# Kernel optimization log

Measured on AMD Instinct MI355X. Metric: run time of the kernel, lower is better.

## Reference

```python
import jax, jax.numpy as jnp
import numpy as np

B, L, NSTATE = 8192, 256, 9


def setup_inputs() -> dict:
    key = jax.random.key(0)
    k1, k2, k3, k4 = jax.random.split(key, 4)
    inputs = jax.random.normal(k1, (B, L, NSTATE), dtype=jnp.float32)
    path = jax.random.randint(k2, (B, L), 0, NSTATE, dtype=jnp.int32)
    # learned CRF params (init'd to zeros in the module; use small random for a
    # non-degenerate reference)
    tran = jax.random.normal(k3, (NSTATE, NSTATE), dtype=jnp.float32) * 0.1
    init = jax.random.normal(k4, (NSTATE,), dtype=jnp.float32) * 0.1
    return {"inputs": inputs, "path": path, "tran": tran, "init": init}


def reference(inputs, path, tran, init):
    # inputs: [B, L, S], path: [B, L], tran: [S, S], init: [S]
    # bio=False -> mask and imask are all zeros (no-op additions).
    # --- gold path score ---
    emit = jnp.take_along_axis(inputs, path[..., None], axis=-1)[..., 0]  # [B, L]
    tran_sc = tran[path[..., :-1], path[..., 1:]]                         # [B, L-1]
    path_scores = emit.sum(-1) + init[path[..., 0]] + tran_sc.sum(-1)     # [B]

    # --- partition function via log-semiring forward recurrence ---
    alpha0 = init + inputs[..., 0, :]                                     # [B, S]

    def step(alpha, x_t):
        # alpha: [B, S] (prev state), x_t: [B, S] (emission at t)
        nxt = alpha[..., :, None] + tran + x_t[..., None, :]              # [B, S, S]
        return jax.nn.logsumexp(nxt, axis=-2), None

    xs = jnp.moveaxis(inputs[..., 1:, :], -2, 0)                          # [L-1, B, S]
    alpha, _ = jax.lax.scan(step, alpha0, xs)
    scores = jax.nn.logsumexp(alpha, axis=-1)                             # [B]
    return scores - path_scores
```

## Files before the change

kernel.cpp:

```cpp
#include <hip/hip_runtime.h>


#define B_N 8192
#define L_N 256
#define SEQ_STRIDE 2304
#define HALF 128
#define SPB 6
#define XW 54
#define XSTRIDE 55
#define NBLK 22
#define PLS 129
#define SPW 16
#define NDIR_BLOCKS (B_N / SPW)

#define LOG2E 1.44269504088896340736f
#define LN2f  0.69314718055994530942f

#define QP1 57
#define QP2 78
#define QP3 147
#define QROT(src, CTRL) \
  __int_as_float(__builtin_amdgcn_mov_dpp(__float_as_int(src), CTRL, 0xf, 0xf, 0))

__device__ __forceinline__ void gl_lds4(const void* g, void* l) {
  __builtin_amdgcn_global_load_lds(
      (const __attribute__((address_space(1))) void*)g,
      (__attribute__((address_space(3))) void*)l, 4, 0, 0);
}

__device__ __forceinline__ float fexp(float x) {
  return __builtin_amdgcn_exp2f(x * LOG2E);
}

__global__ __launch_bounds__(64, 1) void crf_half(
    const float* __restrict__ xg, const int* __restrict__ path,
    const float* __restrict__ tran, const float* __restrict__ initv,
    float* __restrict__ ws)
{
  __shared__ float lx[2][SPW * XSTRIDE];
  __shared__ int   pl[SPW * PLS];
  __shared__ int   pl255[SPW];
  __shared__ float ltran[81];

  const int lane = threadIdx.x;
  const int c = lane & 3;
  const int q = lane >> 2;
  const bool fwd = (int)blockIdx.x < NDIR_BLOCKS;
  const int seq0 = (fwd ? blockIdx.x : blockIdx.x - NDIR_BLOCKS) * SPW;

  for (int i = lane; i < 81; i += 64) ltran[i] = tran[i];

  {
    const int t0 = fwd ? 0 : 127;
#pragma unroll
    for (int r = 0; r < SPW; ++r) {
      const int* g = path + (size_t)(seq0 + r) * L_N + t0 + lane;
      gl_lds4(g,      &pl[r * PLS]);
      gl_lds4(g + 64, &pl[r * PLS + 64]);
    }
  }
  if (!fwd && lane < SPW)
    pl255[lane] = path[(size_t)(seq0 + lane) * L_N + 255];

  if (lane < XW) {
    const int fb = fwd ? 0 : (SEQ_STRIDE - XW);
#pragma unroll
    for (int r = 0; r < SPW; ++r)
      gl_lds4(xg + (size_t)(seq0 + r) * SEQ_STRIDE + fb + lane,
              &lx[0][r * XSTRIDE]);
  }

  float Erot[4][3][3];
#pragma unroll
  for (int r = 0; r < 4; ++r)
#pragma unroll
    for (int k = 0; k < 3; ++k)
#pragma unroll
      for (int i = 0; i < 3; ++i) {
        const int ig = 3 * c + i;
        const int jg = 3 * ((c + r) & 3) + k;
        float v = 0.f;
        if (ig < 9 && jg < 9)
          v = fexp(fwd ? tran[jg * 9 + ig] : tran[ig * 9 + jg]);
        Erot[r][k][i] = v;
      }

  float o[3];
  float emit = 0.f, trn = 0.f;
  int ce = 0, pcur = 0;

  if (!fwd) {
#pragma unroll
    for (int k = 0; k < 3; ++k) o[k] = (c < 3) ? 1.f : 0.f;
    pcur = pl255[q];
  }

  const int myoff = (c == 3) ? 0 : 3 * c;

#pragma unroll 1
  for (int b = 0; b < NBLK; ++b) {
    asm volatile("s_waitcnt vmcnt(0)" ::: "memory");

    if (b + 1 < NBLK && lane < XW) {
      const int fb = fwd ? (b + 1) * XW : (SEQ_STRIDE - XW * (b + 2));
      float* dst = &lx[(b + 1) & 1][0];
#pragma unroll
      for (int r = 0; r < SPW; ++r)
        gl_lds4(xg + (size_t)(seq0 + r) * SEQ_STRIDE + fb + lane,
                dst + r * XSTRIDE);
    }

    const float* lxq = &lx[b & 1][q * XSTRIDE];

    float e[SPB * 3];
#pragma unroll
    for (int tt = 0; tt < SPB; ++tt)
#pragma unroll
      for (int k = 0; k < 3; ++k)
        e[tt * 3 + k] = fexp(lxq[tt * 9 + myoff + k]);

    if (fwd) {
#pragma unroll
      for (int kk = 0; kk < SPB; ++kk) {
        const int t = b * SPB + kk;
        if (t < HALF) {
          if (t == 0) {
#pragma unroll
            for (int k = 0; k < 3; ++k)
              o[k] = (c < 3) ? fexp(initv[3 * c + k] + lxq[myoff + k]) : 0.f;
            pcur = pl[q * PLS];
            emit = lxq[pcur];
          } else {
            float g[4][3];
#pragma unroll
            for (int k = 0; k < 3; ++k) {
              g[0][k] = o[k];
              g[1][k] = QROT(o[k], QP1);
              g[2][k] = QROT(o[k], QP2);
              g[3][k] = QROT(o[k], QP3);
            }
            if (kk == 0 && b > 0) {
              float m = g[0][0];
#pragma unroll
              for (int r = 0; r < 4; ++r)
#pragma unroll
                for (int k = 0; k < 3; ++k) m = fmaxf(m, g[r][k]);
              const int ex = (int)((__float_as_uint(m) >> 23) & 0xffu) - 126;
              ce += ex;
              const float sc = __uint_as_float((unsigned)(127 - ex) << 23);
#pragma unroll
              for (int r = 0; r < 4; ++r)
#pragma unroll
                for (int k = 0; k < 3; ++k) g[r][k] *= sc;
            }
            float out[3];
#pragma unroll
            for (int i = 0; i < 3; ++i) {
              float a = Erot[0][0][i] * g[0][0];
#pragma unroll
              for (int r = 0; r < 4; ++r)
#pragma unroll
                for (int k = 0; k < 3; ++k)
                  if (r + k > 0) a = fmaf(Erot[r][k][i], g[r][k], a);
              out[i] = a;
            }
            const int p = pl[q * PLS + t];
            emit += lxq[kk * 9 + p];
            trn  += ltran[pcur * 9 + p];
            pcur = p;
#pragma unroll
            for (int i = 0; i < 3; ++i) o[i] = out[i] * e[kk * 3 + i];
          }
        }
      }
    } else {
#pragma unroll
      for (int kk = 0; kk < SPB; ++kk) {
        const int t = 255 - b * SPB - kk;
        if (t >= HALF) {
          const int tt = SPB - 1 - kk;
          float w[3];
#pragma unroll
          for (int k = 0; k < 3; ++k) w[k] = e[tt * 3 + k] * o[k];
          float g[4][3];
#pragma unroll
          for (int k = 0; k < 3; ++k) {
            g[0][k] = w[k];
            g[1][k] = QROT(w[k], QP1);
            g[2][k] = QROT(w[k], QP2);
            g[3][k] = QROT(w[k], QP3);
          }
          if (kk == 0 && b > 0) {
            float m = g[0][0];
#pragma unroll
            for (int r = 0; r < 4; ++r)
#pragma unroll
              for (int k = 0; k < 3; ++k) m = fmaxf(m, g[r][k]);
            const int ex = (int)((__float_as_uint(m) >> 23) & 0xffu) - 126;
            ce += ex;
            const float sc = __uint_as_float((unsigned)(127 - ex) << 23);
#pragma unroll
            for (int r = 0; r < 4; ++r)
#pragma unroll
              for (int k = 0; k < 3; ++k) g[r][k] *= sc;
          }
#pragma unroll
          for (int i = 0; i < 3; ++i) {
            float a = Erot[0][0][i] * g[0][0];
#pragma unroll
            for (int r = 0; r < 4; ++r)
#pragma unroll
              for (int k = 0; k < 3; ++k)
                if (r + k > 0) a = fmaf(Erot[r][k][i], g[r][k], a);
            o[i] = a;
          }
          emit += lxq[tt * 9 + pcur];
          const int pm = pl[q * PLS + (t - 1 - 127)];
          trn += ltran[pm * 9 + pcur];
          pcur = pm;
        }
      }
    }
  }

  const int sq = seq0 + q;
  float* wp = ws + sq;
  if (fwd) {
    if (c < 3) {
#pragma unroll
      for (int k = 0; k < 3; ++k) wp[(3 * c + k) * B_N] = o[k];
    } else {
      wp[9 * B_N] = (float)ce;
      const int p0 = pl[q * PLS];
      wp[10 * B_N] = emit + trn + initv[p0];
    }
  } else {
    if (c < 3) {
#pragma unroll
      for (int k = 0; k < 3; ++k) wp[(11 + 3 * c + k) * B_N] = o[k];
    } else {
      wp[20 * B_N] = (float)ce;
      wp[21 * B_N] = emit + trn;
    }
  }
}

__global__ __launch_bounds__(256) void crf_combine(
    const float* __restrict__ ws, float* __restrict__ out)
{
  const int s = blockIdx.x * 256 + threadIdx.x;
  float dot = 0.f;
#pragma unroll
  for (int i = 0; i < 9; ++i)
    dot = fmaf(ws[i * B_N + s], ws[(11 + i) * B_N + s], dot);
  const float score =
      (__builtin_amdgcn_logf(dot) + ws[9 * B_N + s] + ws[20 * B_N + s]) * LN2f;
  out[s] = score - (ws[10 * B_N + s] + ws[21 * B_N + s]);
}

extern "C" void kernel_launch(void* const* d_in, const int* in_sizes, int n_in,
                              void* d_out, int out_size, void* d_ws, size_t ws_size,
                              hipStream_t stream) {
  (void)in_sizes; (void)n_in; (void)out_size; (void)ws_size;
  const float* xg    = (const float*)d_in[0];
  const int*   path  = (const int*)d_in[1];
  const float* tran  = (const float*)d_in[2];
  const float* initv = (const float*)d_in[3];
  float* ws  = (float*)d_ws;
  float* out = (float*)d_out;

  crf_half<<<2 * NDIR_BLOCKS, 64, 0, stream>>>(xg, path, tran, initv, ws);
  crf_combine<<<B_N / 256, 256, 0, stream>>>(ws, out);
}
```

Before: 133.8 us.

## Fuse forward/backward halves and combine into one kernel with triple-buffered prefetch

Each block now runs two wavefronts, one doing the forward half and one the backward half of the same 16 sequences. The halves are combined through shared memory, which removes the second combine kernel and the workspace round trip. The emission prefetch goes from double to triple buffering, with partial vmcnt waits so loads stay in flight two blocks ahead. The cost is more LDS per block and a block-wide barrier at the end, and the hand-counted vmcnt values must match the number of outstanding loads.

After: 145.5 us. 1.09x slower.

```diff
diff --git a/kernel.cpp b/kernel.cpp
--- a/kernel.cpp
+++ b/kernel.cpp
@@ -11,7 +11,7 @@
 #define NBLK 22
 #define PLS 129
 #define SPW 16
-#define NDIR_BLOCKS (B_N / SPW)
+#define NBLOCKS (B_N / SPW)
 
 #define LOG2E 1.44269504088896340736f
 #define LN2f  0.69314718055994530942f
@@ -22,6 +22,8 @@
 #define QROT(src, CTRL) \
   __int_as_float(__builtin_amdgcn_mov_dpp(__float_as_int(src), CTRL, 0xf, 0xf, 0))
 
+#define WAITV(N) asm volatile("s_waitcnt vmcnt(" #N ")" ::: "memory")
+
 __device__ __forceinline__ void gl_lds4(const void* g, void* l) {
   __builtin_amdgcn_global_load_lds(
       (const __attribute__((address_space(1))) void*)g,
@@ -32,43 +34,25 @@
   return __builtin_amdgcn_exp2f(x * LOG2E);
 }
 
-__global__ __launch_bounds__(64, 1) void crf_half(
+__global__ __launch_bounds__(128, 1) void crf_fused(
     const float* __restrict__ xg, const int* __restrict__ path,
     const float* __restrict__ tran, const float* __restrict__ initv,
-    float* __restrict__ ws)
+    float* __restrict__ out)
 {
-  __shared__ float lx[2][SPW * XSTRIDE];
-  __shared__ int   pl[SPW * PLS];
-  __shared__ int   pl255[SPW];
-  __shared__ float ltran[81];
-
-  const int lane = threadIdx.x;
+  __shared__ float lx[2][3][SPW * XSTRIDE];
+  __shared__ int   pl[2][SPW * PLS];
+  __shared__ float ltran[2][81];
+  __shared__ float comb[2][SPW][11];
+
+  const int tid  = threadIdx.x;
+  const int w    = tid >> 6;
+  const int lane = tid & 63;
   const int c = lane & 3;
   const int q = lane >> 2;
-  const bool fwd = (int)blockIdx.x < NDIR_BLOCKS;
-  const int seq0 = (fwd ? blockIdx.x : blockIdx.x - NDIR_BLOCKS) * SPW;
-
-  for (int i = lane; i < 81; i += 64) ltran[i] = tran[i];
-
-  {
-    const int t0 = fwd ? 0 : 127;
-#pragma unroll
-    for (int r = 0; r < SPW; ++r) {
-      const int* g = path + (size_t)(seq0 + r) * L_N + t0 + lane;
-      gl_lds4(g,      &pl[r * PLS]);
-      gl_lds4(g + 64, &pl[r * PLS + 64]);
-    }
-  }
-  if (!fwd && lane < SPW)
-    pl255[lane] = path[(size_t)(seq0 + lane) * L_N + 255];
-
-  if (lane < XW) {
-    const int fb = fwd ? 0 : (SEQ_STRIDE - XW);
-#pragma unroll
-    for (int r = 0; r < SPW; ++r)
-      gl_lds4(xg + (size_t)(seq0 + r) * SEQ_STRIDE + fb + lane,
-              &lx[0][r * XSTRIDE]);
-  }
+  const bool fwd = (w == 0);
+  const int seq0 = blockIdx.x * SPW;
+
+  for (int i = lane; i < 81; i += 64) ltran[w][i] = tran[i];
 
   float Erot[4][3][3];
 #pragma unroll
@@ -85,32 +69,63 @@
         Erot[r][k][i] = v;
       }
 
+  float iv[3];
+#pragma unroll
+  for (int k = 0; k < 3; ++k) {
+    iv[k] = (fwd && c < 3) ? initv[3 * c + k] : 0.f;
+    asm volatile("" :: "v"(iv[k]));
+  }
+
   float o[3];
   float emit = 0.f, trn = 0.f;
   int ce = 0, pcur = 0;
-
   if (!fwd) {
 #pragma unroll
     for (int k = 0; k < 3; ++k) o[k] = (c < 3) ? 1.f : 0.f;
-    pcur = pl255[q];
-  }
-
+    pcur = path[(size_t)(seq0 + q) * L_N + 255];
+  }
+  asm volatile("" :: "v"(pcur));
   const int myoff = (c == 3) ? 0 : 3 * c;
+
+  {
+    const int t0 = fwd ? 0 : 127;
+#pragma unroll
+    for (int r = 0; r < SPW; ++r) {
+      const int* g = path + (size_t)(seq0 + r) * L_N + t0 + lane;
+      gl_lds4(g,      &pl[w][r * PLS]);
+      gl_lds4(g + 64, &pl[w][r * PLS + 64]);
+    }
+  }
+  if (lane < XW) {
+#pragma unroll
+    for (int wi = 0; wi < 2; ++wi) {
+      const int fb = fwd ? wi * XW : (SEQ_STRIDE - XW * (wi + 1));
+#pragma unroll
+      for (int r = 0; r < SPW; ++r)
+        gl_lds4(xg + (size_t)(seq0 + r) * SEQ_STRIDE + fb + lane,
+                &lx[w][wi][r * XSTRIDE]);
+    }
+  }
 
 #pragma unroll 1
   for (int b = 0; b < NBLK; ++b) {
-    asm volatile("s_waitcnt vmcnt(0)" ::: "memory");
-
-    if (b + 1 < NBLK && lane < XW) {
-      const int fb = fwd ? (b + 1) * XW : (SEQ_STRIDE - XW * (b + 2));
-      float* dst = &lx[(b + 1) & 1][0];
-#pragma unroll
-      for (int r = 0; r < SPW; ++r)
-        gl_lds4(xg + (size_t)(seq0 + r) * SEQ_STRIDE + fb + lane,
-                dst + r * XSTRIDE);
-    }
-
-    const float* lxq = &lx[b & 1][q * XSTRIDE];
+    if (b + 2 < NBLK) {
+      if (lane < XW) {
+        const int fb = fwd ? (b + 2) * XW : (SEQ_STRIDE - XW * (b + 3));
+        float* dst = &lx[w][(b + 2) % 3][0];
+#pragma unroll
+        for (int r = 0; r < SPW; ++r)
+          gl_lds4(xg + (size_t)(seq0 + r) * SEQ_STRIDE + fb + lane,
+                  dst + r * XSTRIDE);
+      }
+      WAITV(32);
+    } else if (b + 1 < NBLK) {
+      WAITV(16);
+    } else {
+      WAITV(0);
+    }
+
+    const float* lxq = &lx[w][b % 3][q * XSTRIDE];
 
     float e[SPB * 3];
 #pragma unroll
@@ -127,8 +142,8 @@
           if (t == 0) {
 #pragma unroll
             for (int k = 0; k < 3; ++k)
-              o[k] = (c < 3) ? fexp(initv[3 * c + k] + lxq[myoff + k]) : 0.f;
-            pcur = pl[q * PLS];
+              o[k] = (c < 3) ? fexp(iv[k] + lxq[myoff + k]) : 0.f;
+            pcur = pl[w][q * PLS];
             emit = lxq[pcur];
           } else {
             float g[4][3];
@@ -153,7 +168,7 @@
 #pragma unroll
                 for (int k = 0; k < 3; ++k) g[r][k] *= sc;
             }
-            float out[3];
+            float out3[3];
 #pragma unroll
             for (int i = 0; i < 3; ++i) {
               float a = Erot[0][0][i] * g[0][0];
@@ -162,14 +177,14 @@
 #pragma unroll
                 for (int k = 0; k < 3; ++k)
                   if (r + k > 0) a = fmaf(Erot[r][k][i], g[r][k], a);
-              out[i] = a;
+              out3[i] = a;
             }
-            const int p = pl[q * PLS + t];
+            const int p = pl[w][q * PLS + t];
             emit += lxq[kk * 9 + p];
-            trn  += ltran[pcur * 9 + p];
+            trn  += ltran[w][pcur * 9 + p];
             pcur = p;
 #pragma unroll
-            for (int i = 0; i < 3; ++i) o[i] = out[i] * e[kk * 3 + i];
+            for (int i = 0; i < 3; ++i) o[i] = out3[i] * e[kk * 3 + i];
           }
         }
       }
@@ -179,16 +194,16 @@
         const int t = 255 - b * SPB - kk;
         if (t >= HALF) {
           const int tt = SPB - 1 - kk;
-          float w[3];
-#pragma unroll
-          for (int k = 0; k < 3; ++k) w[k] = e[tt * 3 + k] * o[k];
+          float wv[3];
+#pragma unroll
+          for (int k = 0; k < 3; ++k) wv[k] = e[tt * 3 + k] * o[k];
           float g[4][3];
 #pragma unroll
           for (int k = 0; k < 3; ++k) {
-            g[0][k] = w[k];
-            g[1][k] = QROT(w[k], QP1);
-            g[2][k] = QROT(w[k], QP2);
-            g[3][k] = QROT(w[k], QP3);
+            g[0][k] = wv[k];
+            g[1][k] = QROT(wv[k], QP1);
+            g[2][k] = QROT(wv[k], QP2);
+            g[3][k] = QROT(wv[k], QP3);
           }
           if (kk == 0 && b > 0) {
             float m = g[0][0];
@@ -215,60 +230,44 @@
             o[i] = a;
           }
           emit += lxq[tt * 9 + pcur];
-          const int pm = pl[q * PLS + (t - 1 - 127)];
-          trn += ltran[pm * 9 + pcur];
+          const int pm = pl[w][q * PLS + (t - 1 - 127)];
+          trn += ltran[w][pm * 9 + pcur];
           pcur = pm;
         }
       }
     }
   }
 
-  const int sq = seq0 + q;
-  float* wp = ws + sq;
-  if (fwd) {
-    if (c < 3) {
-#pragma unroll
-      for (int k = 0; k < 3; ++k) wp[(3 * c + k) * B_N] = o[k];
-    } else {
-      wp[9 * B_N] = (float)ce;
-      const int p0 = pl[q * PLS];
-      wp[10 * B_N] = emit + trn + initv[p0];
-    }
+  if (c < 3) {
+#pragma unroll
+    for (int k = 0; k < 3; ++k) comb[w][q][3 * c + k] = o[k];
   } else {
-    if (c < 3) {
-#pragma unroll
-      for (int k = 0; k < 3; ++k) wp[(11 + 3 * c + k) * B_N] = o[k];
-    } else {
-      wp[20 * B_N] = (float)ce;
-      wp[21 * B_N] = emit + trn;
-    }
-  }
-}
-
-__global__ __launch_bounds__(256) void crf_combine(
-    const float* __restrict__ ws, float* __restrict__ out)
-{
-  const int s = blockIdx.x * 256 + threadIdx.x;
-  float dot = 0.f;
-#pragma unroll
-  for (int i = 0; i < 9; ++i)
-    dot = fmaf(ws[i * B_N + s], ws[(11 + i) * B_N + s], dot);
-  const float score =
-      (__builtin_amdgcn_logf(dot) + ws[9 * B_N + s] + ws[20 * B_N + s]) * LN2f;
-  out[s] = score - (ws[10 * B_N + s] + ws[21 * B_N + s]);
+    comb[w][q][9]  = (float)ce;
+    comb[w][q][10] = fwd ? (emit + trn + initv[pl[w][q * PLS]])
+                         : (emit + trn);
+  }
+  __syncthreads();
+
+  if (tid < SPW) {
+    float dot = 0.f;
+#pragma unroll
+    for (int i = 0; i < 9; ++i)
+      dot = fmaf(comb[0][tid][i], comb[1][tid][i], dot);
+    const float score =
+        (__builtin_amdgcn_logf(dot) + comb[0][tid][9] + comb[1][tid][9]) * LN2f;
+    out[seq0 + tid] = score - (comb[0][tid][10] + comb[1][tid][10]);
+  }
 }
 
 extern "C" void kernel_launch(void* const* d_in, const int* in_sizes, int n_in,
                               void* d_out, int out_size, void* d_ws, size_t ws_size,
                               hipStream_t stream) {
-  (void)in_sizes; (void)n_in; (void)out_size; (void)ws_size;
+  (void)in_sizes; (void)n_in; (void)out_size; (void)d_ws; (void)ws_size;
   const float* xg    = (const float*)d_in[0];
   const int*   path  = (const int*)d_in[1];
   const float* tran  = (const float*)d_in[2];
   const float* initv = (const float*)d_in[3];
-  float* ws  = (float*)d_ws;
   float* out = (float*)d_out;
 
-  crf_half<<<2 * NDIR_BLOCKS, 64, 0, stream>>>(xg, path, tran, initv, ws);
-  crf_combine<<<B_N / 256, 256, 0, stream>>>(ws, out);
-}
+  crf_fused<<<NBLOCKS, 128, 0, stream>>>(xg, path, tran, initv, out);
+}
```

## Map one sequence per lane with full 9x9 matvec instead of DPP quad split

Applied to the files above, without the earlier changes.

Changes the work mapping from four lanes per sequence (exchanging 3-state slices via DPP quad rotations) to one lane per sequence holding all 9 states and the full 9x9 exp-transition matrix in registers. Each wave now handles 64 sequences, so the grid shrinks fourfold and the LDS staging buffers grow accordingly. This removes the DPP cross-lane traffic and the idle fourth lane per quad. In exchange it raises register pressure (81 matrix entries plus state vectors), lengthens the per-lane serial dependency chain, and leaves fewer blocks to hide latency, with more LDS per block.

Result: slower. 158.6 us (+18.5%).

```diff
diff --git a/kernel.cpp b/kernel.cpp
--- a/kernel.cpp
+++ b/kernel.cpp
@@ -10,17 +10,13 @@
 #define XSTRIDE 55
 #define NBLK 22
 #define PLS 129
-#define SPW 16
+#define SPW 64
 #define NDIR_BLOCKS (B_N / SPW)
 
 #define LOG2E 1.44269504088896340736f
 #define LN2f  0.69314718055994530942f
 
-#define QP1 57
-#define QP2 78
-#define QP3 147
-#define QROT(src, CTRL) \
-  __int_as_float(__builtin_amdgcn_mov_dpp(__float_as_int(src), CTRL, 0xf, 0xf, 0))
+#define WAITV0 asm volatile("s_waitcnt vmcnt(0)" ::: "memory")
 
 __device__ __forceinline__ void gl_lds4(const void* g, void* l) {
   __builtin_amdgcn_global_load_lds(
@@ -39,137 +35,109 @@
 {
   __shared__ float lx[2][SPW * XSTRIDE];
   __shared__ int   pl[SPW * PLS];
-  __shared__ int   pl255[SPW];
   __shared__ float ltran[81];
 
   const int lane = threadIdx.x;
-  const int c = lane & 3;
-  const int q = lane >> 2;
   const bool fwd = (int)blockIdx.x < NDIR_BLOCKS;
   const int seq0 = (fwd ? blockIdx.x : blockIdx.x - NDIR_BLOCKS) * SPW;
 
   for (int i = lane; i < 81; i += 64) ltran[i] = tran[i];
 
+  float E[9][9];
+#pragma unroll
+  for (int i = 0; i < 9; ++i)
+#pragma unroll
+    for (int j = 0; j < 9; ++j)
+      E[i][j] = fexp(fwd ? tran[j * 9 + i] : tran[i * 9 + j]);
+
+  float iv[9];
+#pragma unroll
+  for (int j = 0; j < 9; ++j) iv[j] = initv[j];
+
+  float a[9];
+  float emit = 0.f, trn = 0.f;
+  int ce = 0, pcur = 0;
+  if (!fwd) {
+#pragma unroll
+    for (int j = 0; j < 9; ++j) a[j] = 1.f;
+    pcur = path[(size_t)(seq0 + lane) * L_N + 255];
+  }
+  asm volatile("" :: "v"(pcur));
+
   {
     const int t0 = fwd ? 0 : 127;
-#pragma unroll
+#pragma unroll 4
     for (int r = 0; r < SPW; ++r) {
       const int* g = path + (size_t)(seq0 + r) * L_N + t0 + lane;
       gl_lds4(g,      &pl[r * PLS]);
       gl_lds4(g + 64, &pl[r * PLS + 64]);
     }
   }
-  if (!fwd && lane < SPW)
-    pl255[lane] = path[(size_t)(seq0 + lane) * L_N + 255];
-
   if (lane < XW) {
     const int fb = fwd ? 0 : (SEQ_STRIDE - XW);
-#pragma unroll
+#pragma unroll 4
     for (int r = 0; r < SPW; ++r)
       gl_lds4(xg + (size_t)(seq0 + r) * SEQ_STRIDE + fb + lane,
               &lx[0][r * XSTRIDE]);
   }
 
-  float Erot[4][3][3];
-#pragma unroll
-  for (int r = 0; r < 4; ++r)
-#pragma unroll
-    for (int k = 0; k < 3; ++k)
-#pragma unroll
-      for (int i = 0; i < 3; ++i) {
-        const int ig = 3 * c + i;
-        const int jg = 3 * ((c + r) & 3) + k;
-        float v = 0.f;
-        if (ig < 9 && jg < 9)
-          v = fexp(fwd ? tran[jg * 9 + ig] : tran[ig * 9 + jg]);
-        Erot[r][k][i] = v;
-      }
-
-  float o[3];
-  float emit = 0.f, trn = 0.f;
-  int ce = 0, pcur = 0;
-
-  if (!fwd) {
-#pragma unroll
-    for (int k = 0; k < 3; ++k) o[k] = (c < 3) ? 1.f : 0.f;
-    pcur = pl255[q];
-  }
-
-  const int myoff = (c == 3) ? 0 : 3 * c;
+  const int* plr = &pl[lane * PLS];
 
 #pragma unroll 1
   for (int b = 0; b < NBLK; ++b) {
-    asm volatile("s_waitcnt vmcnt(0)" ::: "memory");
+    WAITV0;
 
     if (b + 1 < NBLK && lane < XW) {
       const int fb = fwd ? (b + 1) * XW : (SEQ_STRIDE - XW * (b + 2));
       float* dst = &lx[(b + 1) & 1][0];
-#pragma unroll
+#pragma unroll 4
       for (int r = 0; r < SPW; ++r)
         gl_lds4(xg + (size_t)(seq0 + r) * SEQ_STRIDE + fb + lane,
                 dst + r * XSTRIDE);
     }
 
-    const float* lxq = &lx[b & 1][q * XSTRIDE];
-
-    float e[SPB * 3];
-#pragma unroll
-    for (int tt = 0; tt < SPB; ++tt)
-#pragma unroll
-      for (int k = 0; k < 3; ++k)
-        e[tt * 3 + k] = fexp(lxq[tt * 9 + myoff + k]);
+    const float* lxr = &lx[b & 1][lane * XSTRIDE];
 
     if (fwd) {
 #pragma unroll
       for (int kk = 0; kk < SPB; ++kk) {
         const int t = b * SPB + kk;
         if (t < HALF) {
+          float xv[9], ee[9];
+#pragma unroll
+          for (int j = 0; j < 9; ++j) xv[j] = lxr[kk * 9 + j];
+#pragma unroll
+          for (int j = 0; j < 9; ++j) ee[j] = fexp(xv[j]);
           if (t == 0) {
 #pragma unroll
-            for (int k = 0; k < 3; ++k)
-              o[k] = (c < 3) ? fexp(initv[3 * c + k] + lxq[myoff + k]) : 0.f;
-            pcur = pl[q * PLS];
-            emit = lxq[pcur];
+            for (int j = 0; j < 9; ++j) a[j] = fexp(iv[j] + xv[j]);
+            pcur = plr[0];
+            emit += lxr[pcur];
           } else {
-            float g[4][3];
-#pragma unroll
-            for (int k = 0; k < 3; ++k) {
-              g[0][k] = o[k];
-              g[1][k] = QROT(o[k], QP1);
-              g[2][k] = QROT(o[k], QP2);
-              g[3][k] = QROT(o[k], QP3);
-            }
             if (kk == 0 && b > 0) {
-              float m = g[0][0];
-#pragma unroll
-              for (int r = 0; r < 4; ++r)
-#pragma unroll
-                for (int k = 0; k < 3; ++k) m = fmaxf(m, g[r][k]);
+              float m = a[0];
+#pragma unroll
+              for (int j = 1; j < 9; ++j) m = fmaxf(m, a[j]);
               const int ex = (int)((__float_as_uint(m) >> 23) & 0xffu) - 126;
               ce += ex;
               const float sc = __uint_as_float((unsigned)(127 - ex) << 23);
 #pragma unroll
-              for (int r = 0; r < 4; ++r)
-#pragma unroll
-                for (int k = 0; k < 3; ++k) g[r][k] *= sc;
+              for (int j = 0; j < 9; ++j) a[j] *= sc;
             }
-            float out[3];
-#pragma unroll
-            for (int i = 0; i < 3; ++i) {
-              float a = Erot[0][0][i] * g[0][0];
-#pragma unroll
-              for (int r = 0; r < 4; ++r)
-#pragma unroll
-                for (int k = 0; k < 3; ++k)
-                  if (r + k > 0) a = fmaf(Erot[r][k][i], g[r][k], a);
-              out[i] = a;
+            float outv[9];
+#pragma unroll
+            for (int i = 0; i < 9; ++i) {
+              float acc = E[i][0] * a[0];
+#pragma unroll
+              for (int j = 1; j < 9; ++j) acc = fmaf(E[i][j], a[j], acc);
+              outv[i] = acc;
             }
-            const int p = pl[q * PLS + t];
-            emit += lxq[kk * 9 + p];
+            const int p = plr[t];
+            emit += lxr[kk * 9 + p];
             trn  += ltran[pcur * 9 + p];
             pcur = p;
 #pragma unroll
-            for (int i = 0; i < 3; ++i) o[i] = out[i] * e[kk * 3 + i];
+            for (int i = 0; i < 9; ++i) a[i] = outv[i] * ee[i];
           }
         }
       }
@@ -179,69 +147,54 @@
         const int t = 255 - b * SPB - kk;
         if (t >= HALF) {
           const int tt = SPB - 1 - kk;
-          float w[3];
-#pragma unroll
-          for (int k = 0; k < 3; ++k) w[k] = e[tt * 3 + k] * o[k];
-          float g[4][3];
-#pragma unroll
-          for (int k = 0; k < 3; ++k) {
-            g[0][k] = w[k];
-            g[1][k] = QROT(w[k], QP1);
-            g[2][k] = QROT(w[k], QP2);
-            g[3][k] = QROT(w[k], QP3);
-          }
+          float xv[9], ee[9], wv[9];
+#pragma unroll
+          for (int j = 0; j < 9; ++j) xv[j] = lxr[tt * 9 + j];
+#pragma unroll
+          for (int j = 0; j < 9; ++j) ee[j] = fexp(xv[j]);
+#pragma unroll
+          for (int j = 0; j < 9; ++j) wv[j] = ee[j] * a[j];
           if (kk == 0 && b > 0) {
-            float m = g[0][0];
-#pragma unroll
-            for (int r = 0; r < 4; ++r)
-#pragma unroll
-              for (int k = 0; k < 3; ++k) m = fmaxf(m, g[r][k]);
+            float m = wv[0];
+#pragma unroll
+            for (int j = 1; j < 9; ++j) m = fmaxf(m, wv[j]);
             const int ex = (int)((__float_as_uint(m) >> 23) & 0xffu) - 126;
             ce += ex;
             const float sc = __uint_as_float((unsigned)(127 - ex) << 23);
 #pragma unroll
-            for (int r = 0; r < 4; ++r)
-#pragma unroll
-              for (int k = 0; k < 3; ++k) g[r][k] *= sc;
+            for (int j = 0; j < 9; ++j) wv[j] *= sc;
           }
-#pragma unroll
-          for (int i = 0; i < 3; ++i) {
-            float a = Erot[0][0][i] * g[0][0];
-#pragma unroll
-            for (int r = 0; r < 4; ++r)
-#pragma unroll
-              for (int k = 0; k < 3; ++k)
-                if (r + k > 0) a = fmaf(Erot[r][k][i], g[r][k], a);
-            o[i] = a;
+          float outv[9];
+#pragma unroll
+          for (int i = 0; i < 9; ++i) {
+            float acc = E[i][0] * wv[0];
+#pragma unroll
+            for (int j = 1; j < 9; ++j) acc = fmaf(E[i][j], wv[j], acc);
+            outv[i] = acc;
           }
-          emit += lxq[tt * 9 + pcur];
-          const int pm = pl[q * PLS + (t - 1 - 127)];
+          emit += lxr[tt * 9 + pcur];
+          const int pm = plr[t - 128];
           trn += ltran[pm * 9 + pcur];
           pcur = pm;
+#pragma unroll
+          for (int i = 0; i < 9; ++i) a[i] = outv[i];
         }
       }
     }
   }
 
-  const int sq = seq0 + q;
+  const int sq = seq0 + lane;
   float* wp = ws + sq;
   if (fwd) {
-    if (c < 3) {
-#pragma unroll
-      for (int k = 0; k < 3; ++k) wp[(3 * c + k) * B_N] = o[k];
-    } else {
-      wp[9 * B_N] = (float)ce;
-      const int p0 = pl[q * PLS];
-      wp[10 * B_N] = emit + trn + initv[p0];
-    }
+#pragma unroll
+    for (int i = 0; i < 9; ++i) wp[i * B_N] = a[i];
+    wp[9 * B_N] = (float)ce;
+    wp[10 * B_N] = emit + trn + initv[plr[0]];
   } else {
-    if (c < 3) {
-#pragma unroll
-      for (int k = 0; k < 3; ++k) wp[(11 + 3 * c + k) * B_N] = o[k];
-    } else {
-      wp[20 * B_N] = (float)ce;
-      wp[21 * B_N] = emit + trn;
-    }
+#pragma unroll
+    for (int i = 0; i < 9; ++i) wp[(11 + i) * B_N] = a[i];
+    wp[20 * B_N] = (float)ce;
+    wp[21 * B_N] = emit + trn;
   }
 }
 
```

## Peel first and last blocks, prefetch path indices, batch gold-path gathers

Applied to the files above, without the earlier changes.

Restructures the time loop by peeling the first block (init) and the tail block (2 steps), which removes the per-step t<HALF and t==0 branches from the steady-state loop. The six path indices for the next block are read from LDS one block ahead, and the emission and transition gathers for the gold-path score are batched up front, taking them off the recurrence's dependent chain. The init vector is loaded into registers before the loop. The cost is more code size and register pressure.

Measured after the change: 126.5 us. 1.06x faster.

```diff
diff --git a/kernel.cpp b/kernel.cpp
--- a/kernel.cpp
+++ b/kernel.cpp
@@ -22,6 +22,8 @@
 #define QROT(src, CTRL) \
   __int_as_float(__builtin_amdgcn_mov_dpp(__float_as_int(src), CTRL, 0xf, 0xf, 0))
 
+#define WAITV0 asm volatile("s_waitcnt vmcnt(0)" ::: "memory")
+
 __device__ __forceinline__ void gl_lds4(const void* g, void* l) {
   __builtin_amdgcn_global_load_lds(
       (const __attribute__((address_space(1))) void*)g,
@@ -31,6 +33,116 @@
 __device__ __forceinline__ float fexp(float x) {
   return __builtin_amdgcn_exp2f(x * LOG2E);
 }
+
+#define FWD_STEP_BODY(KK, DO_RESC)                                          \
+  do {                                                                      \
+    float g[4][3];                                                          \
+    _Pragma("unroll") for (int k = 0; k < 3; ++k) {                         \
+      g[0][k] = o[k];                                                       \
+      g[1][k] = QROT(o[k], QP1);                                            \
+      g[2][k] = QROT(o[k], QP2);                                            \
+      g[3][k] = QROT(o[k], QP3);                                            \
+    }                                                                       \
+    if (DO_RESC) {                                                          \
+      float m = g[0][0];                                                    \
+      _Pragma("unroll") for (int r = 0; r < 4; ++r)                         \
+        _Pragma("unroll") for (int k = 0; k < 3; ++k)                       \
+          m = fmaxf(m, g[r][k]);                                            \
+      const int ex = (int)((__float_as_uint(m) >> 23) & 0xffu) - 126;       \
+      ce += ex;                                                             \
+      const float sc = __uint_as_float((unsigned)(127 - ex) << 23);         \
+      _Pragma("unroll") for (int r = 0; r < 4; ++r)                         \
+        _Pragma("unroll") for (int k = 0; k < 3; ++k)                       \
+          g[r][k] *= sc;                                                    \
+    }                                                                       \
+    float out3[3];                                                          \
+    _Pragma("unroll") for (int i = 0; i < 3; ++i) {                         \
+      float a = Erot[0][0][i] * g[0][0];                                    \
+      _Pragma("unroll") for (int r = 0; r < 4; ++r)                         \
+        _Pragma("unroll") for (int k = 0; k < 3; ++k)                       \
+          if (r + k > 0) a = fmaf(Erot[r][k][i], g[r][k], a);               \
+      out3[i] = a;                                                          \
+    }                                                                       \
+    _Pragma("unroll") for (int i = 0; i < 3; ++i)                           \
+      o[i] = out3[i] * e[(KK) * 3 + i];                                     \
+  } while (0)
+
+#define BWD_STEP_BODY(KK, DO_RESC)                                          \
+  do {                                                                      \
+    const int tt_ = 5 - (KK);                                               \
+    float wv[3];                                                            \
+    _Pragma("unroll") for (int k = 0; k < 3; ++k)                           \
+      wv[k] = e[tt_ * 3 + k] * o[k];                                        \
+    float g[4][3];                                                          \
+    _Pragma("unroll") for (int k = 0; k < 3; ++k) {                         \
+      g[0][k] = wv[k];                                                      \
+      g[1][k] = QROT(wv[k], QP1);                                           \
+      g[2][k] = QROT(wv[k], QP2);                                           \
+      g[3][k] = QROT(wv[k], QP3);                                           \
+    }                                                                       \
+    if (DO_RESC) {                                                          \
+      float m = g[0][0];                                                    \
+      _Pragma("unroll") for (int r = 0; r < 4; ++r)                         \
+        _Pragma("unroll") for (int k = 0; k < 3; ++k)                       \
+          m = fmaxf(m, g[r][k]);                                            \
+      const int ex = (int)((__float_as_uint(m) >> 23) & 0xffu) - 126;       \
+      ce += ex;                                                             \
+      const float sc = __uint_as_float((unsigned)(127 - ex) << 23);         \
+      _Pragma("unroll") for (int r = 0; r < 4; ++r)                         \
+        _Pragma("unroll") for (int k = 0; k < 3; ++k)                       \
+          g[r][k] *= sc;                                                    \
+    }                                                                       \
+    float out3[3];                                                          \
+    _Pragma("unroll") for (int i = 0; i < 3; ++i) {                         \
+      float a = Erot[0][0][i] * g[0][0];                                    \
+      _Pragma("unroll") for (int r = 0; r < 4; ++r)                         \
+        _Pragma("unroll") for (int k = 0; k < 3; ++k)                       \
+          if (r + k > 0) a = fmaf(Erot[r][k][i], g[r][k], a);               \
+      out3[i] = a;                                                          \
+    }                                                                       \
+    _Pragma("unroll") for (int i = 0; i < 3; ++i) o[i] = out3[i];           \
+  } while (0)
+
+#define PREFETCH_WIN(NB)                                                    \
+  if (lane < XW) {                                                          \
+    const int fb = fwd ? (NB) * XW : (SEQ_STRIDE - XW * ((NB) + 1));        \
+    float* dst = &lx[(NB) & 1][0];                                          \
+    _Pragma("unroll") for (int r = 0; r < SPW; ++r)                         \
+      gl_lds4(xg + (size_t)(seq0 + r) * SEQ_STRIDE + fb + lane,             \
+              dst + r * XSTRIDE);                                           \
+  }
+
+#define EBATCH(T0, T1)                                                      \
+  _Pragma("unroll") for (int tt = (T0); tt <= (T1); ++tt)                   \
+    _Pragma("unroll") for (int k = 0; k < 3; ++k)                           \
+      e[tt * 3 + k] = fexp(lxq[tt * 9 + myoff + k]);
+
+#define EMTR_FWD(N)                                                         \
+  _Pragma("unroll") for (int kk = 0; kk < (N); ++kk) {                      \
+    em[kk] = lxq[kk * 9 + pc6[kk]];                                         \
+    const int pp = kk ? pc6[kk - 1] : pcur;                                 \
+    tr[kk] = ltran[pp * 9 + pc6[kk]];                                       \
+  }
+
+#define EMTR_BWD(N)                                                         \
+  _Pragma("unroll") for (int kk = 0; kk < (N); ++kk) {                      \
+    const int pc = kk ? pc6[kk - 1] : pcur;                                 \
+    em[kk] = lxq[(5 - kk) * 9 + pc];                                        \
+    tr[kk] = ltran[pc6[kk] * 9 + pc];                                       \
+  }
+
+#define PREREAD_PN(TBN)                                                     \
+  if (fwd) {                                                                \
+    _Pragma("unroll") for (int kk = 0; kk < SPB; ++kk) {                    \
+      int t = (TBN) + kk; if (t > HALF - 1) t = HALF - 1;                   \
+      pn6[kk] = plr[t];                                                     \
+    }                                                                       \
+  } else {                                                                  \
+    _Pragma("unroll") for (int kk = 0; kk < SPB; ++kk) {                    \
+      int idx = 127 - (TBN) - kk; if (idx < 0) idx = 0;                     \
+      pn6[kk] = plr[idx];                                                   \
+    }                                                                       \
+  }
 
 __global__ __launch_bounds__(64, 1) void crf_half(
     const float* __restrict__ xg, const int* __restrict__ path,
@@ -61,7 +173,6 @@
   }
   if (!fwd && lane < SPW)
     pl255[lane] = path[(size_t)(seq0 + lane) * L_N + 255];
-
   if (lane < XW) {
     const int fb = fwd ? 0 : (SEQ_STRIDE - XW);
 #pragma unroll
@@ -85,142 +196,125 @@
         Erot[r][k][i] = v;
       }
 
+  float iv[3];
+#pragma unroll
+  for (int k = 0; k < 3; ++k) {
+    iv[k] = (fwd && c < 3) ? initv[3 * c + k] : 0.f;
+    asm volatile("" :: "v"(iv[k]));
+  }
+
   float o[3];
   float emit = 0.f, trn = 0.f;
   int ce = 0, pcur = 0;
-
   if (!fwd) {
 #pragma unroll
     for (int k = 0; k < 3; ++k) o[k] = (c < 3) ? 1.f : 0.f;
-    pcur = pl255[q];
   }
 
   const int myoff = (c == 3) ? 0 : 3 * c;
+  const int* plr = &pl[q * PLS];
+
+  WAITV0;
+  if (!fwd) pcur = pl255[q];
+
+  int pc6[SPB];
+  if (fwd) {
+#pragma unroll
+    for (int kk = 0; kk < SPB; ++kk) pc6[kk] = plr[kk];
+  } else {
+#pragma unroll
+    for (int kk = 0; kk < SPB; ++kk) pc6[kk] = plr[127 - kk];
+  }
+
+  {
+    PREFETCH_WIN(1)
+    const float* lxq = &lx[0][q * XSTRIDE];
+    float e[SPB * 3];
+    EBATCH(0, 5)
+    float em[SPB], tr[SPB];
+    int pn6[SPB];
+    if (fwd) { EMTR_FWD(6) } else { EMTR_BWD(6) }
+    PREREAD_PN(SPB)
+    if (fwd) {
+#pragma unroll
+      for (int k = 0; k < 3; ++k)
+        o[k] = (c < 3) ? fexp(iv[k] + lxq[myoff + k]) : 0.f;
+      FWD_STEP_BODY(1, false);
+      FWD_STEP_BODY(2, false);
+      FWD_STEP_BODY(3, false);
+      FWD_STEP_BODY(4, false);
+      FWD_STEP_BODY(5, false);
+#pragma unroll
+      for (int kk = 0; kk < 6; ++kk) emit += em[kk];
+#pragma unroll
+      for (int kk = 1; kk < 6; ++kk) trn += tr[kk];
+    } else {
+      BWD_STEP_BODY(0, false);
+      BWD_STEP_BODY(1, false);
+      BWD_STEP_BODY(2, false);
+      BWD_STEP_BODY(3, false);
+      BWD_STEP_BODY(4, false);
+      BWD_STEP_BODY(5, false);
+#pragma unroll
+      for (int kk = 0; kk < 6; ++kk) { emit += em[kk]; trn += tr[kk]; }
+    }
+    pcur = pc6[SPB - 1];
+#pragma unroll
+    for (int kk = 0; kk < SPB; ++kk) pc6[kk] = pn6[kk];
+  }
 
 #pragma unroll 1
-  for (int b = 0; b < NBLK; ++b) {
-    asm volatile("s_waitcnt vmcnt(0)" ::: "memory");
-
-    if (b + 1 < NBLK && lane < XW) {
-      const int fb = fwd ? (b + 1) * XW : (SEQ_STRIDE - XW * (b + 2));
-      float* dst = &lx[(b + 1) & 1][0];
-#pragma unroll
-      for (int r = 0; r < SPW; ++r)
-        gl_lds4(xg + (size_t)(seq0 + r) * SEQ_STRIDE + fb + lane,
-                dst + r * XSTRIDE);
-    }
-
+  for (int b = 1; b <= 20; ++b) {
+    const int tb = b * SPB;
+    WAITV0;
+    PREFETCH_WIN(b + 1)
     const float* lxq = &lx[b & 1][q * XSTRIDE];
-
     float e[SPB * 3];
-#pragma unroll
-    for (int tt = 0; tt < SPB; ++tt)
-#pragma unroll
-      for (int k = 0; k < 3; ++k)
-        e[tt * 3 + k] = fexp(lxq[tt * 9 + myoff + k]);
-
+    EBATCH(0, 5)
+    float em[SPB], tr[SPB];
+    int pn6[SPB];
+    if (fwd) { EMTR_FWD(6) } else { EMTR_BWD(6) }
+    PREREAD_PN(tb + SPB)
     if (fwd) {
-#pragma unroll
-      for (int kk = 0; kk < SPB; ++kk) {
-        const int t = b * SPB + kk;
-        if (t < HALF) {
-          if (t == 0) {
-#pragma unroll
-            for (int k = 0; k < 3; ++k)
-              o[k] = (c < 3) ? fexp(initv[3 * c + k] + lxq[myoff + k]) : 0.f;
-            pcur = pl[q * PLS];
-            emit = lxq[pcur];
-          } else {
-            float g[4][3];
-#pragma unroll
-            for (int k = 0; k < 3; ++k) {
-              g[0][k] = o[k];
-              g[1][k] = QROT(o[k], QP1);
-              g[2][k] = QROT(o[k], QP2);
-              g[3][k] = QROT(o[k], QP3);
-            }
-            if (kk == 0 && b > 0) {
-              float m = g[0][0];
-#pragma unroll
-              for (int r = 0; r < 4; ++r)
-#pragma unroll
-                for (int k = 0; k < 3; ++k) m = fmaxf(m, g[r][k]);
-              const int ex = (int)((__float_as_uint(m) >> 23) & 0xffu) - 126;
-              ce += ex;
-              const float sc = __uint_as_float((unsigned)(127 - ex) << 23);
-#pragma unroll
-              for (int r = 0; r < 4; ++r)
-#pragma unroll
-                for (int k = 0; k < 3; ++k) g[r][k] *= sc;
-            }
-            float out[3];
-#pragma unroll
-            for (int i = 0; i < 3; ++i) {
-              float a = Erot[0][0][i] * g[0][0];
-#pragma unroll
-              for (int r = 0; r < 4; ++r)
-#pragma unroll
-                for (int k = 0; k < 3; ++k)
-                  if (r + k > 0) a = fmaf(Erot[r][k][i], g[r][k], a);
-              out[i] = a;
-            }
-            const int p = pl[q * PLS + t];
-            emit += lxq[kk * 9 + p];
-            trn  += ltran[pcur * 9 + p];
-            pcur = p;
-#pragma unroll
-            for (int i = 0; i < 3; ++i) o[i] = out[i] * e[kk * 3 + i];
-          }
-        }
-      }
-    } else {
-#pragma unroll
-      for (int kk = 0; kk < SPB; ++kk) {
-        const int t = 255 - b * SPB - kk;
-        if (t >= HALF) {
-          const int tt = SPB - 1 - kk;
-          float w[3];
-#pragma unroll
-          for (int k = 0; k < 3; ++k) w[k] = e[tt * 3 + k] * o[k];
-          float g[4][3];
-#pragma unroll
-          for (int k = 0; k < 3; ++k) {
-            g[0][k] = w[k];
-            g[1][k] = QROT(w[k], QP1);
-            g[2][k] = QROT(w[k], QP2);
-            g[3][k] = QROT(w[k], QP3);
-          }
-          if (kk == 0 && b > 0) {
-            float m = g[0][0];
-#pragma unroll
-            for (int r = 0; r < 4; ++r)
-#pragma unroll
-              for (int k = 0; k < 3; ++k) m = fmaxf(m, g[r][k]);
-            const int ex = (int)((__float_as_uint(m) >> 23) & 0xffu) - 126;
-            ce += ex;
-            const float sc = __uint_as_float((unsigned)(127 - ex) << 23);
-#pragma unroll
-            for (int r = 0; r < 4; ++r)
-#pragma unroll
-              for (int k = 0; k < 3; ++k) g[r][k] *= sc;
-          }
-#pragma unroll
-          for (int i = 0; i < 3; ++i) {
-            float a = Erot[0][0][i] * g[0][0];
-#pragma unroll
-            for (int r = 0; r < 4; ++r)
-#pragma unroll
-              for (int k = 0; k < 3; ++k)
-                if (r + k > 0) a = fmaf(Erot[r][k][i], g[r][k], a);
-            o[i] = a;
-          }
-          emit += lxq[tt * 9 + pcur];
-          const int pm = pl[q * PLS + (t - 1 - 127)];
-          trn += ltran[pm * 9 + pcur];
-          pcur = pm;
-        }
-      }
-    }
+      FWD_STEP_BODY(0, true);
+      FWD_STEP_BODY(1, false);
+      FWD_STEP_BODY(2, false);
+      FWD_STEP_BODY(3, false);
+      FWD_STEP_BODY(4, false);
+      FWD_STEP_BODY(5, false);
+    } else {
+      BWD_STEP_BODY(0, true);
+      BWD_STEP_BODY(1, false);
+      BWD_STEP_BODY(2, false);
+      BWD_STEP_BODY(3, false);
+      BWD_STEP_BODY(4, false);
+      BWD_STEP_BODY(5, false);
+    }
+#pragma unroll
+    for (int kk = 0; kk < 6; ++kk) { emit += em[kk]; trn += tr[kk]; }
+    pcur = pc6[SPB - 1];
+#pragma unroll
+    for (int kk = 0; kk < SPB; ++kk) pc6[kk] = pn6[kk];
+  }
+
+  {
+    WAITV0;
+    const float* lxq = &lx[1][q * XSTRIDE];
+    float e[SPB * 3];
+    float em[SPB], tr[SPB];
+    if (fwd) {
+      EBATCH(0, 1)
+      EMTR_FWD(2)
+      FWD_STEP_BODY(0, true);
+      FWD_STEP_BODY(1, false);
+    } else {
+      EBATCH(4, 5)
+      EMTR_BWD(2)
+      BWD_STEP_BODY(0, true);
+      BWD_STEP_BODY(1, false);
+    }
+#pragma unroll
+    for (int kk = 0; kk < 2; ++kk) { emit += em[kk]; trn += tr[kk]; }
   }
 
   const int sq = seq0 + q;
@@ -231,8 +325,7 @@
       for (int k = 0; k < 3; ++k) wp[(3 * c + k) * B_N] = o[k];
     } else {
       wp[9 * B_N] = (float)ce;
-      const int p0 = pl[q * PLS];
-      wp[10 * B_N] = emit + trn + initv[p0];
+      wp[10 * B_N] = emit + trn + initv[plr[0]];
     }
   } else {
     if (c < 3) {
```
